# Kernel tuning notes

Hardware: AMD Instinct MI355X
Metric: run time of the kernel (lower is better)

The kernel has to match this reference:

```python
import jax, jax.numpy as jnp
import numpy as np

B, IN_DIM, OUT_DIM, N = 8, 128, 128, 256
BN_EPS = 1e-5


def setup_inputs() -> dict:
    key = jax.random.key(0)
    ks = jax.random.split(key, 6)
    A = jax.random.normal(ks[0], (B, IN_DIM, N), dtype=jnp.float32)
    ini_p = float(np.sqrt(3.0 / OUT_DIM / IN_DIM))
    ini_qk = float(np.sqrt(1.0 / OUT_DIM / IN_DIM))
    P1 = jax.random.uniform(ks[1], (OUT_DIM, IN_DIM), minval=-ini_p, maxval=ini_p, dtype=jnp.float32)
    P2 = jax.random.uniform(ks[2], (OUT_DIM, IN_DIM), minval=-ini_p, maxval=ini_p, dtype=jnp.float32)
    q = jax.random.uniform(ks[3], (OUT_DIM, IN_DIM), minval=-ini_qk, maxval=ini_qk, dtype=jnp.float32)
    k = jax.random.uniform(ks[4], (OUT_DIM, IN_DIM), minval=-ini_qk, maxval=ini_qk, dtype=jnp.float32)
    gamma = jnp.ones((OUT_DIM,), dtype=jnp.float32)
    beta = jnp.zeros((OUT_DIM,), dtype=jnp.float32)
    return {"A": A, "P1": P1, "P2": P2, "q": q, "k": k,
            "gamma": gamma, "beta": beta,
            "permutation_size1": N, "BATCH_SIZE": B}


def reference(A, P1, P2, q, k, gamma, beta, permutation_size1, BATCH_SIZE):
    # A: [B, in_dim, n]; params [out_dim, in_dim]
    A1 = jnp.einsum('oi,bin->bon', P1, A)            # [B, C, n]
    Q = jnp.einsum('oi,bin->bon', q, A)              # [B, C, n]
    K = jnp.einsum('oi,bin->bon', k, A)              # [B, C, n]
    # Rank-1 outer product per (b, c): Alpha[b,c,i,j] = Q[b,c,i] * K[b,c,j]
    Alpha = Q[..., :, None] * K[..., None, :]        # [B, C, n, n]
    row_norm = jnp.linalg.norm(Alpha, axis=3, keepdims=True)  # [B, C, n, 1]
    Alpha_norm = jnp.abs(Alpha) / row_norm
    V = jnp.einsum('oi,bin->bon', P2, A)             # [B, C, n]
    Y = jnp.einsum('bcij,bcj->bci', Alpha_norm, V)   # [B, C, n]
    out = A1 + V + 0.1 * Y
    out = jax.nn.relu(out)
    # BatchNorm1d (training mode): normalize per channel over (B, n)
    mean = out.mean(axis=(0, 2), keepdims=True)
    var = out.var(axis=(0, 2), keepdims=True)
    out = (out - mean) * jax.lax.rsqrt(var + BN_EPS)
    out = out * gamma[None, :, None] + beta[None, :, None]
    return out
```

## Files before the change

### kernel.cpp

```cpp
#include <hip/hip_runtime.h>
#include <math.h>

#define BB   8
#define IND  128
#define OUTD 128
#define NN   256
#define NQ   64
#define BN_EPS 1e-5f
#define PSTR 13

__global__ __launch_bounds__(1024) void layer1dpe_fused(
    const float* __restrict__ A,
    const float* __restrict__ P1,
    const float* __restrict__ P2,
    const float* __restrict__ kw,
    const float* __restrict__ gamma,
    const float* __restrict__ beta,
    float* __restrict__ out)
{
    const int c = blockIdx.x;
    const int x = threadIdx.x;
    const int b = threadIdx.y;
    const int z = threadIdx.z;

    __shared__ float w1[IND], w2[IND], wk[IND];
    __shared__ float part[BB][NQ][PSTR];
    __shared__ float red[BB][2];

    {
        const int tid = (z * BB + b) * 64 + x;
        if (tid < 128)      w1[tid]       = P1[c * IND + tid];
        else if (tid < 256) w2[tid - 128] = P2[c * IND + tid - 128];
        else if (tid < 384) wk[tid - 256] = kw[c * IND + tid - 256];
    }
    __syncthreads();

    const float4* __restrict__ A4 = (const float4*)A;
    float a1[4], vv[4], kv[4];
    #pragma unroll
    for (int j = 0; j < 4; ++j) { a1[j] = 0.f; vv[j] = 0.f; kv[j] = 0.f; }

    const int ibase = z * 64;
    #pragma unroll
    for (int blk = 0; blk < 8; ++blk) {
        float4 cur[8];
        #pragma unroll
        for (int j = 0; j < 8; ++j)
            cur[j] = A4[(b * IND + ibase + blk * 8 + j) * NQ + x];
        #pragma unroll
        for (int j = 0; j < 8; ++j) {
            const int iw = ibase + blk * 8 + j;
            const float wa = w1[iw], wb = w2[iw], wc = wk[iw];
            a1[0] = fmaf(wa, cur[j].x, a1[0]); a1[1] = fmaf(wa, cur[j].y, a1[1]);
            a1[2] = fmaf(wa, cur[j].z, a1[2]); a1[3] = fmaf(wa, cur[j].w, a1[3]);
            vv[0] = fmaf(wb, cur[j].x, vv[0]); vv[1] = fmaf(wb, cur[j].y, vv[1]);
            vv[2] = fmaf(wb, cur[j].z, vv[2]); vv[3] = fmaf(wb, cur[j].w, vv[3]);
            kv[0] = fmaf(wc, cur[j].x, kv[0]); kv[1] = fmaf(wc, cur[j].y, kv[1]);
            kv[2] = fmaf(wc, cur[j].z, kv[2]); kv[3] = fmaf(wc, cur[j].w, kv[3]);
        }
    }

    if (z == 1) {
        #pragma unroll
        for (int j = 0; j < 4; ++j) {
            part[b][x][j]     = a1[j];
            part[b][x][4 + j] = vv[j];
            part[b][x][8 + j] = kv[j];
        }
    }
    __syncthreads();

    float p[4];
    float bnsum = 0.f, bnsq = 0.f;
    if (z == 0) {
        #pragma unroll
        for (int j = 0; j < 4; ++j) {
            a1[j] += part[b][x][j];
            vv[j] += part[b][x][4 + j];
            kv[j] += part[b][x][8 + j];
        }
        float s2 = 0.f, sv = 0.f;
        #pragma unroll
        for (int j = 0; j < 4; ++j) {
            s2 = fmaf(kv[j], kv[j], s2);
            sv = fmaf(fabsf(kv[j]), vv[j], sv);
        }
        #pragma unroll
        for (int off = 32; off >= 1; off >>= 1) {
            s2 += __shfl_xor(s2, off, 64);
            sv += __shfl_xor(sv, off, 64);
        }
        const float y = sv / sqrtf(s2);

        #pragma unroll
        for (int j = 0; j < 4; ++j) {
            float t = a1[j] + vv[j] + 0.1f * y;
            t = fmaxf(t, 0.f);
            p[j] = t;
            bnsum += t;
            bnsq  = fmaf(t, t, bnsq);
        }
        #pragma unroll
        for (int off = 32; off >= 1; off >>= 1) {
            bnsum += __shfl_xor(bnsum, off, 64);
            bnsq  += __shfl_xor(bnsq,  off, 64);
        }
        if (x == 0) { red[b][0] = bnsum; red[b][1] = bnsq; }
    }
    __syncthreads();

    if (z == 0) {
        float tsum = 0.f, tsq = 0.f;
        #pragma unroll
        for (int w = 0; w < BB; ++w) { tsum += red[w][0]; tsq += red[w][1]; }

        const float inv   = 1.f / (float)(BB * NN);
        const float mean  = tsum * inv;
        const float var   = tsq * inv - mean * mean;
        const float scale = gamma[c] * rsqrtf(var + BN_EPS);
        const float shift = beta[c] - mean * scale;

        float4* __restrict__ out4 = (float4*)out;
        out4[(b * OUTD + c) * NQ + x] = make_float4(
            fmaf(p[0], scale, shift), fmaf(p[1], scale, shift),
            fmaf(p[2], scale, shift), fmaf(p[3], scale, shift));
    }
}

extern "C" void kernel_launch(void* const* d_in, const int* in_sizes, int n_in,
                              void* d_out, int out_size, void* d_ws, size_t ws_size,
                              hipStream_t stream) {
    const float* A     = (const float*)d_in[0];
    const float* P1    = (const float*)d_in[1];
    const float* P2    = (const float*)d_in[2];
    const float* kw    = (const float*)d_in[4];
    const float* gamma = (const float*)d_in[5];
    const float* beta  = (const float*)d_in[6];
    float* out = (float*)d_out;

    dim3 block(64, 8, 2);
    layer1dpe_fused<<<OUTD, block, 0, stream>>>(A, P1, P2, kw, gamma, beta, out);
}
```

Baseline: 79.63 us.

## Split fused kernel into projection kernel and batchnorm kernel for more parallelism

Replaces the single 128-block kernel (1024 threads each, batch in threadIdx.y, input dim split across z) with two kernels. The first launches 128x8 blocks of 64 threads, each doing the full input-dim projection for one (channel, batch) pair and writing pre-BN values and partial sums to workspace. The second reduces the partials and applies the normalization. This spreads the work over many more small blocks to fill more CUs, at the cost of an extra launch and a round trip of the intermediate through global memory.

```diff
diff --git a/kernel.cpp b/kernel.cpp
--- a/kernel.cpp
+++ b/kernel.cpp
@@ -7,50 +7,38 @@
 #define NN   256
 #define NQ   64
 #define BN_EPS 1e-5f
-#define PSTR 13
 
-__global__ __launch_bounds__(1024) void layer1dpe_fused(
+__global__ __launch_bounds__(64) void k1_proj(
     const float* __restrict__ A,
     const float* __restrict__ P1,
     const float* __restrict__ P2,
     const float* __restrict__ kw,
-    const float* __restrict__ gamma,
-    const float* __restrict__ beta,
-    float* __restrict__ out)
+    float* __restrict__ pbuf,
+    float* __restrict__ bnp)
 {
     const int c = blockIdx.x;
+    const int b = blockIdx.y;
     const int x = threadIdx.x;
-    const int b = threadIdx.y;
-    const int z = threadIdx.z;
 
-    __shared__ float w1[IND], w2[IND], wk[IND];
-    __shared__ float part[BB][NQ][PSTR];
-    __shared__ float red[BB][2];
+    const float4* __restrict__ A4 = (const float4*)A + (size_t)b * IND * NQ;
+    const float* __restrict__ w1 = P1 + c * IND;
+    const float* __restrict__ w2 = P2 + c * IND;
+    const float* __restrict__ w3 = kw + c * IND;
 
-    {
-        const int tid = (z * BB + b) * 64 + x;
-        if (tid < 128)      w1[tid]       = P1[c * IND + tid];
-        else if (tid < 256) w2[tid - 128] = P2[c * IND + tid - 128];
-        else if (tid < 384) wk[tid - 256] = kw[c * IND + tid - 256];
-    }
-    __syncthreads();
+    float a1[4] = {0.f, 0.f, 0.f, 0.f};
+    float vv[4] = {0.f, 0.f, 0.f, 0.f};
+    float kv[4] = {0.f, 0.f, 0.f, 0.f};
 
-    const float4* __restrict__ A4 = (const float4*)A;
-    float a1[4], vv[4], kv[4];
     #pragma unroll
-    for (int j = 0; j < 4; ++j) { a1[j] = 0.f; vv[j] = 0.f; kv[j] = 0.f; }
-
-    const int ibase = z * 64;
-    #pragma unroll
-    for (int blk = 0; blk < 8; ++blk) {
+    for (int blk = 0; blk < 16; ++blk) {
         float4 cur[8];
         #pragma unroll
         for (int j = 0; j < 8; ++j)
-            cur[j] = A4[(b * IND + ibase + blk * 8 + j) * NQ + x];
+            cur[j] = A4[(blk * 8 + j) * NQ + x];
         #pragma unroll
         for (int j = 0; j < 8; ++j) {
-            const int iw = ibase + blk * 8 + j;
-            const float wa = w1[iw], wb = w2[iw], wc = wk[iw];
+            const int i = blk * 8 + j;
+            const float wa = w1[i], wb = w2[i], wc = w3[i];
             a1[0] = fmaf(wa, cur[j].x, a1[0]); a1[1] = fmaf(wa, cur[j].y, a1[1]);
             a1[2] = fmaf(wa, cur[j].z, a1[2]); a1[3] = fmaf(wa, cur[j].w, a1[3]);
             vv[0] = fmaf(wb, cur[j].x, vv[0]); vv[1] = fmaf(wb, cur[j].y, vv[1]);
@@ -60,71 +48,72 @@
         }
     }
 
-    if (z == 1) {
-        #pragma unroll
-        for (int j = 0; j < 4; ++j) {
-            part[b][x][j]     = a1[j];
-            part[b][x][4 + j] = vv[j];
-            part[b][x][8 + j] = kv[j];
-        }
+    float s2 = 0.f, sv = 0.f;
+    #pragma unroll
+    for (int j = 0; j < 4; ++j) {
+        s2 = fmaf(kv[j], kv[j], s2);
+        sv = fmaf(fabsf(kv[j]), vv[j], sv);
     }
-    __syncthreads();
+    #pragma unroll
+    for (int off = 32; off >= 1; off >>= 1) {
+        s2 += __shfl_xor(s2, off, 64);
+        sv += __shfl_xor(sv, off, 64);
+    }
+    const float y = sv / sqrtf(s2);
 
     float p[4];
     float bnsum = 0.f, bnsq = 0.f;
-    if (z == 0) {
-        #pragma unroll
-        for (int j = 0; j < 4; ++j) {
-            a1[j] += part[b][x][j];
-            vv[j] += part[b][x][4 + j];
-            kv[j] += part[b][x][8 + j];
-        }
-        float s2 = 0.f, sv = 0.f;
-        #pragma unroll
-        for (int j = 0; j < 4; ++j) {
-            s2 = fmaf(kv[j], kv[j], s2);
-            sv = fmaf(fabsf(kv[j]), vv[j], sv);
-        }
-        #pragma unroll
-        for (int off = 32; off >= 1; off >>= 1) {
-            s2 += __shfl_xor(s2, off, 64);
-            sv += __shfl_xor(sv, off, 64);
-        }
-        const float y = sv / sqrtf(s2);
+    #pragma unroll
+    for (int j = 0; j < 4; ++j) {
+        float t = a1[j] + vv[j] + 0.1f * y;
+        t = fmaxf(t, 0.f);
+        p[j] = t;
+        bnsum += t;
+        bnsq  = fmaf(t, t, bnsq);
+    }
+    #pragma unroll
+    for (int off = 32; off >= 1; off >>= 1) {
+        bnsum += __shfl_xor(bnsum, off, 64);
+        bnsq  += __shfl_xor(bnsq,  off, 64);
+    }
 
-        #pragma unroll
-        for (int j = 0; j < 4; ++j) {
-            float t = a1[j] + vv[j] + 0.1f * y;
-            t = fmaxf(t, 0.f);
-            p[j] = t;
-            bnsum += t;
-            bnsq  = fmaf(t, t, bnsq);
-        }
-        #pragma unroll
-        for (int off = 32; off >= 1; off >>= 1) {
-            bnsum += __shfl_xor(bnsum, off, 64);
-            bnsq  += __shfl_xor(bnsq,  off, 64);
-        }
-        if (x == 0) { red[b][0] = bnsum; red[b][1] = bnsq; }
+    float4* __restrict__ p4 = (float4*)pbuf;
+    p4[((size_t)b * OUTD + c) * NQ + x] = make_float4(p[0], p[1], p[2], p[3]);
+    if (x == 0) {
+        bnp[c * BB + b]              = bnsum;
+        bnp[OUTD * BB + c * BB + b]  = bnsq;
     }
-    __syncthreads();
+}
 
-    if (z == 0) {
-        float tsum = 0.f, tsq = 0.f;
-        #pragma unroll
-        for (int w = 0; w < BB; ++w) { tsum += red[w][0]; tsq += red[w][1]; }
+__global__ __launch_bounds__(512) void k2_bn(
+    const float* __restrict__ pbuf,
+    const float* __restrict__ bnp,
+    const float* __restrict__ gamma,
+    const float* __restrict__ beta,
+    float* __restrict__ out)
+{
+    const int c = blockIdx.x;
+    const int x = threadIdx.x;
+    const int b = threadIdx.y;
 
-        const float inv   = 1.f / (float)(BB * NN);
-        const float mean  = tsum * inv;
-        const float var   = tsq * inv - mean * mean;
-        const float scale = gamma[c] * rsqrtf(var + BN_EPS);
-        const float shift = beta[c] - mean * scale;
+    float tsum = 0.f, tsq = 0.f;
+    #pragma unroll
+    for (int w = 0; w < BB; ++w) {
+        tsum += bnp[c * BB + w];
+        tsq  += bnp[OUTD * BB + c * BB + w];
+    }
+    const float inv   = 1.f / (float)(BB * NN);
+    const float mean  = tsum * inv;
+    const float var   = tsq * inv - mean * mean;
+    const float scale = gamma[c] * rsqrtf(var + BN_EPS);
+    const float shift = beta[c] - mean * scale;
 
-        float4* __restrict__ out4 = (float4*)out;
-        out4[(b * OUTD + c) * NQ + x] = make_float4(
-            fmaf(p[0], scale, shift), fmaf(p[1], scale, shift),
-            fmaf(p[2], scale, shift), fmaf(p[3], scale, shift));
-    }
+    const float4* __restrict__ p4 = (const float4*)pbuf;
+    float4* __restrict__ out4 = (float4*)out;
+    const size_t idx = ((size_t)b * OUTD + c) * NQ + x;
+    const float4 p = p4[idx];
+    out4[idx] = make_float4(fmaf(p.x, scale, shift), fmaf(p.y, scale, shift),
+                            fmaf(p.z, scale, shift), fmaf(p.w, scale, shift));
 }
 
 extern "C" void kernel_launch(void* const* d_in, const int* in_sizes, int n_in,
@@ -138,6 +127,11 @@
     const float* beta  = (const float*)d_in[6];
     float* out = (float*)d_out;
 
-    dim3 block(64, 8, 2);
-    layer1dpe_fused<<<OUTD, block, 0, stream>>>(A, P1, P2, kw, gamma, beta, out);
+    float* pbuf = (float*)d_ws;
+    float* bnp  = (float*)((char*)d_ws + (size_t)BB * OUTD * NN * sizeof(float));
+
+    dim3 g1(OUTD, BB);
+    k1_proj<<<g1, 64, 0, stream>>>(A, P1, P2, kw, pbuf, bnp);
+    dim3 b2(64, BB);
+    k2_bn<<<OUTD, b2, 0, stream>>>(pbuf, bnp, gamma, beta, out);
 }
```

New measurement: 77.88 us. 1.02x faster.
